# Kernel tuning notes

Hardware: AMD Instinct MI355X
Metric: run time of the kernel (lower is better)

## Reference

```python
import jax, jax.numpy as jnp
import numpy as np

K = 6                 # color-coding parameter; K-1 message-passing steps
N = 50000             # num nodes
E = 1600000           # num edges (avg degree 32)
F = 384               # num_node_features = K * 2**K


def setup_inputs() -> dict:
    key = jax.random.key(0)
    k1, k2, k3, k4, k5 = jax.random.split(key, 5)
    s = 1.0 / np.sqrt(F)
    x = jax.random.normal(k1, (N, F), dtype=jnp.float32)
    edge_index = jax.random.randint(k2, (2, E), 0, N, dtype=jnp.int32)
    batch = jnp.zeros((N,), dtype=jnp.int32)  # unused by forward, kept for signature parity
    W_rel = jax.random.normal(k3, (F, F), dtype=jnp.float32) * s   # GraphConv lin_rel weight
    W_root = jax.random.normal(k4, (F, F), dtype=jnp.float32) * s  # GraphConv lin_root weight
    W_lin = jax.random.normal(k5, (1, F), dtype=jnp.float32) * s   # readout linear (no bias)
    return {"x": x, "edge_index": edge_index, "batch": batch,
            "W_rel": W_rel, "W_root": W_root, "W_lin": W_lin}


def reference(x, edge_index, batch, W_rel, W_root, W_lin):
    src = edge_index[0]
    dst = edge_index[1]
    # K-1 iterations of PyG GraphConv(aggr='add', bias=False) + relu:
    #   out = segment_sum(x[src] -> dst) @ W_rel^T + x @ W_root^T
    for _ in range(K - 1):
        agg = jax.ops.segment_sum(x[src], dst, num_segments=N)  # [N, F]
        x = jax.nn.relu(agg @ W_rel.T + x @ W_root.T)
    # readout: Linear(F, 1, bias=False)
    return x @ W_lin.T  # [N, 1]
```

## Files before the change

### kernel.cpp

```cpp
#include <hip/hip_runtime.h>
#include <hip/hip_bf16.h>

#define NN 50000
#define EE 1600000
#define FF 384
#define MPAD 50048
#define NITER 5

typedef unsigned int u32;
typedef unsigned short u16;
typedef __attribute__((ext_vector_type(8))) short short8;
typedef __attribute__((ext_vector_type(4))) float f32x4;

typedef const __attribute__((address_space(1))) void* gptr_t;
typedef __attribute__((address_space(3))) void* lptr_t;

__device__ __forceinline__ float bf_lo(u32 u) {
  u32 v = u << 16;
  return __builtin_bit_cast(float, v);
}
__device__ __forceinline__ float bf_hi(u32 u) {
  u32 v = u & 0xFFFF0000u;
  return __builtin_bit_cast(float, v);
}
__device__ __forceinline__ u32 f2bf(float f) {
  u32 u = __builtin_bit_cast(u32, f);
  return (u + 0x7FFFu + ((u >> 16) & 1u)) >> 16;
}
__device__ __forceinline__ u32 pack2(float lo, float hi) {
  return f2bf(lo) | (f2bf(hi) << 16);
}
__device__ __forceinline__ void load16_lds(const void* g, void* l) {
  __builtin_amdgcn_global_load_lds((gptr_t)g, (lptr_t)l, 16, 0, 0);
}

__global__ void hist_kernel(const int* __restrict__ dst, int* __restrict__ cnt) {
  int e = blockIdx.x * 256 + threadIdx.x;
  if (e < EE) atomicAdd(&cnt[dst[e]], 1);
}

__global__ void scan_kernel(const int* __restrict__ cnt, int* __restrict__ row_start,
                            int* __restrict__ cursor) {
  __shared__ int part[256];
  __shared__ int pre[256];
  const int CH = (NN + 255) / 256;
  int t = threadIdx.x;
  int lo = t * CH;
  int hi = lo + CH; if (hi > NN) hi = NN;
  int s = 0;
  for (int i = lo; i < hi; ++i) s += cnt[i];
  part[t] = s;
  __syncthreads();
  if (t == 0) {
    int run = 0;
    for (int i = 0; i < 256; ++i) { pre[i] = run; run += part[i]; }
  }
  __syncthreads();
  int run = pre[t];
  for (int i = lo; i < hi; ++i) {
    row_start[i] = run;
    cursor[i] = run;
    run += cnt[i];
  }
  if (lo < NN && hi == NN) row_start[NN] = run;
}

__global__ void scatter_kernel(const int* __restrict__ src, const int* __restrict__ dst,
                               int* __restrict__ cursor, int* __restrict__ col) {
  int e = blockIdx.x * 256 + threadIdx.x;
  if (e < EE) {
    int d = dst[e];
    int p = atomicAdd(&cursor[d], 1);
    col[p] = src[e];
  }
}

__global__ void convert_x_kernel(const float* __restrict__ xin, u16* __restrict__ xout) {
  size_t i = ((size_t)blockIdx.x * 256 + threadIdx.x) * 4;
  if (i >= (size_t)NN * FF) return;
  float4 f = *(const float4*)(xin + i);
  u32 o0 = pack2(f.x, f.y);
  u32 o1 = pack2(f.z, f.w);
  u32* q = (u32*)(xout + i);
  q[0] = o0; q[1] = o1;
}

__global__ void build_bt_kernel(const float* __restrict__ Wr, const float* __restrict__ Wt,
                                u16* __restrict__ Bt) {
  int i = blockIdx.x * 256 + threadIdx.x;
  if (i >= FF * 2 * FF) return;
  int n = i / (2 * FF);
  int k = i - n * (2 * FF);
  float v = (k < FF) ? Wr[n * FF + k] : Wt[n * FF + (k - FF)];
  Bt[i] = (u16)f2bf(v);
}

__global__ void spmm_kernel(const u16* __restrict__ x, const int* __restrict__ rs,
                            const int* __restrict__ col, u16* __restrict__ agg) {
  int row = blockIdx.x * 4 + (threadIdx.x >> 6);
  int lane = threadIdx.x & 63;
  if (row >= NN) return;
  int j0 = rs[row], j1 = rs[row + 1];
  float a0 = 0.f, a1 = 0.f, a2 = 0.f, a3 = 0.f, a4 = 0.f, a5 = 0.f;
  int j = j0;
  for (; j + 2 <= j1; j += 2) {
    int s0 = col[j], s1 = col[j + 1];
    const u32* p0 = (const u32*)(x + (size_t)s0 * FF) + lane * 3;
    const u32* p1 = (const u32*)(x + (size_t)s1 * FF) + lane * 3;
    u32 u0 = p0[0], u1 = p0[1], u2 = p0[2];
    u32 v0 = p1[0], v1 = p1[1], v2 = p1[2];
    a0 += bf_lo(u0); a1 += bf_hi(u0);
    a2 += bf_lo(u1); a3 += bf_hi(u1);
    a4 += bf_lo(u2); a5 += bf_hi(u2);
    a0 += bf_lo(v0); a1 += bf_hi(v0);
    a2 += bf_lo(v1); a3 += bf_hi(v1);
    a4 += bf_lo(v2); a5 += bf_hi(v2);
  }
  if (j < j1) {
    int s0 = col[j];
    const u32* p0 = (const u32*)(x + (size_t)s0 * FF) + lane * 3;
    u32 u0 = p0[0], u1 = p0[1], u2 = p0[2];
    a0 += bf_lo(u0); a1 += bf_hi(u0);
    a2 += bf_lo(u1); a3 += bf_hi(u1);
    a4 += bf_lo(u2); a5 += bf_hi(u2);
  }
  u32* q = (u32*)(agg + (size_t)row * FF) + lane * 3;
  q[0] = pack2(a0, a1);
  q[1] = pack2(a2, a3);
  q[2] = pack2(a4, a5);
}

__global__ __launch_bounds__(256) void gemm_kernel(
    const u16* __restrict__ Aagg, const u16* __restrict__ Ax,
    const u16* __restrict__ Bt, u16* __restrict__ Xout) {
  __shared__ __align__(16) u16 As[128 * 64];
  __shared__ __align__(16) u16 Bs[128 * 64];
  const int m0 = blockIdx.x * 128;
  const int n0 = blockIdx.y * 128;
  const int tid = threadIdx.x;
  const int lane = tid & 63;
  const int w = tid >> 6;
  const int wr = w >> 1, wc = w & 1;

  const int sr = lane >> 3;
  const int sbc = (lane & 7) << 4;

  f32x4 acc[4][4] = {};

  for (int kt = 0; kt < 12; ++kt) {
    const u16* Asrc = (kt < 6) ? Aagg : Ax;
    const int kbA = (kt < 6 ? kt : kt - 6) << 7;
    const int kbB = kt << 7;
#pragma unroll
    for (int i = 0; i < 4; ++i) {
      const int r = w * 32 + i * 8 + sr;
      const int swz = sbc ^ ((r & 7) << 4);
      load16_lds((const char*)Asrc + (size_t)(m0 + r) * 768 + kbA + swz,
                 &As[(w * 32 + i * 8) * 64]);
      load16_lds((const char*)Bt + (size_t)(n0 + r) * 1536 + kbB + swz,
                 &Bs[(w * 32 + i * 8) * 64]);
    }
    __syncthreads();
#pragma unroll
    for (int ks = 0; ks < 2; ++ks) {
      short8 af[4], bfm[4];
#pragma unroll
      for (int mi = 0; mi < 4; ++mi) {
        const int r = wr * 64 + mi * 16 + (lane & 15);
        const int bc = (ks * 64 + ((lane >> 4) << 4)) ^ ((r & 7) << 4);
        af[mi] = *(const short8*)((const char*)As + r * 128 + bc);
      }
#pragma unroll
      for (int ni = 0; ni < 4; ++ni) {
        const int r = wc * 64 + ni * 16 + (lane & 15);
        const int bc = (ks * 64 + ((lane >> 4) << 4)) ^ ((r & 7) << 4);
        bfm[ni] = *(const short8*)((const char*)Bs + r * 128 + bc);
      }
#pragma unroll
      for (int mi = 0; mi < 4; ++mi)
#pragma unroll
        for (int ni = 0; ni < 4; ++ni)
          acc[mi][ni] = __builtin_amdgcn_mfma_f32_16x16x32_bf16(af[mi], bfm[ni], acc[mi][ni], 0, 0, 0);
    }
    __syncthreads();
  }

#pragma unroll
  for (int mi = 0; mi < 4; ++mi) {
#pragma unroll
    for (int r = 0; r < 4; ++r) {
      const int row = m0 + wr * 64 + mi * 16 + ((lane >> 4) << 2) + r;
      u16* orow = Xout + (size_t)row * FF + n0 + wc * 64 + (lane & 15);
#pragma unroll
      for (int ni = 0; ni < 4; ++ni) {
        float v = fmaxf(acc[mi][ni][r], 0.0f);
        orow[ni * 16] = (u16)f2bf(v);
      }
    }
  }
}

__global__ void readout_kernel(const u16* __restrict__ x, const float* __restrict__ wl,
                               float* __restrict__ out) {
  int row = blockIdx.x * 4 + (threadIdx.x >> 6);
  int lane = threadIdx.x & 63;
  if (row >= NN) return;
  const u32* p = (const u32*)(x + (size_t)row * FF) + lane * 3;
  u32 u0 = p[0], u1 = p[1], u2 = p[2];
  const float* w = wl + lane * 6;
  float s = bf_lo(u0) * w[0] + bf_hi(u0) * w[1] +
            bf_lo(u1) * w[2] + bf_hi(u1) * w[3] +
            bf_lo(u2) * w[4] + bf_hi(u2) * w[5];
#pragma unroll
  for (int off = 32; off > 0; off >>= 1) s += __shfl_down(s, off, 64);
  if (lane == 0) out[row] = s;
}

extern "C" void kernel_launch(void* const* d_in, const int* in_sizes, int n_in,
                              void* d_out, int out_size, void* d_ws, size_t ws_size,
                              hipStream_t stream) {
  const float* x_in = (const float*)d_in[0];
  const int* ei = (const int*)d_in[1];
  const float* W_rel = (const float*)d_in[3];
  const float* W_root = (const float*)d_in[4];
  const float* W_lin = (const float*)d_in[5];
  float* out = (float*)d_out;

  char* ws = (char*)d_ws;
  int* cnt = (int*)(ws);
  int* row_start = (int*)(ws + 200064);
  int* cursor = (int*)(ws + 400128);
  int* col = (int*)(ws + 600192);
  u16* Bt = (u16*)(ws + 7000192);
  u16* agg = (u16*)(ws + 7590016);
  u16* x0 = (u16*)(ws + 46026880);
  u16* x1 = (u16*)(ws + 84463744);
  if (ws_size < (size_t)122900608) return;

  const int* esrc = ei;
  const int* edst = ei + EE;

  hipMemsetAsync(cnt, 0, NN * sizeof(int), stream);
  hipMemsetAsync(agg + (size_t)NN * FF, 0, (size_t)(MPAD - NN) * FF * sizeof(u16), stream);
  hipMemsetAsync(x0 + (size_t)NN * FF, 0, (size_t)(MPAD - NN) * FF * sizeof(u16), stream);
  hipMemsetAsync(x1 + (size_t)NN * FF, 0, (size_t)(MPAD - NN) * FF * sizeof(u16), stream);

  hist_kernel<<<EE / 256, 256, 0, stream>>>(edst, cnt);
  scan_kernel<<<1, 256, 0, stream>>>(cnt, row_start, cursor);
  scatter_kernel<<<EE / 256, 256, 0, stream>>>(esrc, edst, cursor, col);
  convert_x_kernel<<<(NN * FF / 4 + 255) / 256, 256, 0, stream>>>(x_in, x0);
  build_bt_kernel<<<(FF * 2 * FF + 255) / 256, 256, 0, stream>>>(W_rel, W_root, Bt);

  u16* xs = x0;
  u16* xd = x1;
  for (int t = 0; t < NITER; ++t) {
    spmm_kernel<<<NN / 4, 256, 0, stream>>>(xs, row_start, col, agg);
    gemm_kernel<<<dim3(MPAD / 128, FF / 128), 256, 0, stream>>>(agg, xs, Bt, xd);
    u16* tmp = xs; xs = xd; xd = tmp;
  }
  readout_kernel<<<NN / 4, 256, 0, stream>>>(xs, W_lin, out);
}
```

Before: 1.397 ms.

## Vectorize SpMM gathers, parallelize CSR scan, and swap GEMM grid ordering

The SpMM kernel now gathers each neighbor row with 16-byte loads on 48 lanes instead of three 4-byte loads on 64 lanes, and unrolls four edges per iteration to keep more loads in flight. The CSR scan replaces the serial single-thread prefix with wave shuffles and int4 vector reads and writes. The GEMM grid puts the N tiles on the fast-varying dimension, so the three column blocks that share an A row tile run close together and reuse it in L2. Leaving 16 lanes idle in SpMM gives up some occupancy in exchange for wider, fewer memory transactions.

```diff
diff --git a/kernel.cpp b/kernel.cpp
--- a/kernel.cpp
+++ b/kernel.cpp
@@ -41,28 +41,31 @@
 
 __global__ void scan_kernel(const int* __restrict__ cnt, int* __restrict__ row_start,
                             int* __restrict__ cursor) {
-  __shared__ int part[256];
-  __shared__ int pre[256];
-  const int CH = (NN + 255) / 256;
+  __shared__ int wsum[4];
+  const int CH = 196;
   int t = threadIdx.x;
   int lo = t * CH;
   int hi = lo + CH; if (hi > NN) hi = NN;
   int s = 0;
-  for (int i = lo; i < hi; ++i) s += cnt[i];
-  part[t] = s;
+  int n4 = (hi - lo) >> 2;
+  const int4* p = (const int4*)(cnt + lo);
+  for (int i = 0; i < n4; ++i) { int4 c = p[i]; s += c.x + c.y + c.z + c.w; }
+  int lane = t & 63, w = t >> 6;
+  int v = s;
+  for (int d = 1; d < 64; d <<= 1) { int u = __shfl_up(v, d, 64); if (lane >= d) v += u; }
+  if (lane == 63) wsum[w] = v;
   __syncthreads();
-  if (t == 0) {
-    int run = 0;
-    for (int i = 0; i < 256; ++i) { pre[i] = run; run += part[i]; }
-  }
-  __syncthreads();
-  int run = pre[t];
-  for (int i = lo; i < hi; ++i) {
-    row_start[i] = run;
-    cursor[i] = run;
-    run += cnt[i];
-  }
-  if (lo < NN && hi == NN) row_start[NN] = run;
+  int run = v - s;
+  for (int i = 0; i < w; ++i) run += wsum[i];
+  int4* q1 = (int4*)(row_start + lo);
+  int4* q2 = (int4*)(cursor + lo);
+  for (int k = 0; k < n4; ++k) {
+    int4 c = p[k];
+    int4 o; o.x = run; o.y = run + c.x; o.z = o.y + c.y; o.w = o.z + c.z;
+    run = o.w + c.w;
+    q1[k] = o; q2[k] = o;
+  }
+  if (hi == NN && lo < NN) row_start[NN] = run;
 }
 
 __global__ void scatter_kernel(const int* __restrict__ src, const int* __restrict__ dst,
@@ -95,39 +98,46 @@
   Bt[i] = (u16)f2bf(v);
 }
 
+#define ACC8(u)                                  \
+  a0 += bf_lo(u.x); a1 += bf_hi(u.x);            \
+  a2 += bf_lo(u.y); a3 += bf_hi(u.y);            \
+  a4 += bf_lo(u.z); a5 += bf_hi(u.z);            \
+  a6 += bf_lo(u.w); a7 += bf_hi(u.w);
+
 __global__ void spmm_kernel(const u16* __restrict__ x, const int* __restrict__ rs,
                             const int* __restrict__ col, u16* __restrict__ agg) {
   int row = blockIdx.x * 4 + (threadIdx.x >> 6);
   int lane = threadIdx.x & 63;
   if (row >= NN) return;
   int j0 = rs[row], j1 = rs[row + 1];
-  float a0 = 0.f, a1 = 0.f, a2 = 0.f, a3 = 0.f, a4 = 0.f, a5 = 0.f;
+  float a0 = 0.f, a1 = 0.f, a2 = 0.f, a3 = 0.f;
+  float a4 = 0.f, a5 = 0.f, a6 = 0.f, a7 = 0.f;
+  const bool active = lane < 48;
+  const int off = lane * 4;
   int j = j0;
-  for (; j + 2 <= j1; j += 2) {
-    int s0 = col[j], s1 = col[j + 1];
-    const u32* p0 = (const u32*)(x + (size_t)s0 * FF) + lane * 3;
-    const u32* p1 = (const u32*)(x + (size_t)s1 * FF) + lane * 3;
-    u32 u0 = p0[0], u1 = p0[1], u2 = p0[2];
-    u32 v0 = p1[0], v1 = p1[1], v2 = p1[2];
-    a0 += bf_lo(u0); a1 += bf_hi(u0);
-    a2 += bf_lo(u1); a3 += bf_hi(u1);
-    a4 += bf_lo(u2); a5 += bf_hi(u2);
-    a0 += bf_lo(v0); a1 += bf_hi(v0);
-    a2 += bf_lo(v1); a3 += bf_hi(v1);
-    a4 += bf_lo(v2); a5 += bf_hi(v2);
-  }
-  if (j < j1) {
+  for (; j + 4 <= j1; j += 4) {
+    int s0 = col[j], s1 = col[j + 1], s2 = col[j + 2], s3 = col[j + 3];
+    if (active) {
+      uint4 u0 = *(const uint4*)((const u32*)(x + (size_t)s0 * FF) + off);
+      uint4 u1 = *(const uint4*)((const u32*)(x + (size_t)s1 * FF) + off);
+      uint4 u2 = *(const uint4*)((const u32*)(x + (size_t)s2 * FF) + off);
+      uint4 u3 = *(const uint4*)((const u32*)(x + (size_t)s3 * FF) + off);
+      ACC8(u0); ACC8(u1); ACC8(u2); ACC8(u3);
+    }
+  }
+  for (; j < j1; ++j) {
     int s0 = col[j];
-    const u32* p0 = (const u32*)(x + (size_t)s0 * FF) + lane * 3;
-    u32 u0 = p0[0], u1 = p0[1], u2 = p0[2];
-    a0 += bf_lo(u0); a1 += bf_hi(u0);
-    a2 += bf_lo(u1); a3 += bf_hi(u1);
-    a4 += bf_lo(u2); a5 += bf_hi(u2);
-  }
-  u32* q = (u32*)(agg + (size_t)row * FF) + lane * 3;
-  q[0] = pack2(a0, a1);
-  q[1] = pack2(a2, a3);
-  q[2] = pack2(a4, a5);
+    if (active) {
+      uint4 u0 = *(const uint4*)((const u32*)(x + (size_t)s0 * FF) + off);
+      ACC8(u0);
+    }
+  }
+  if (active) {
+    uint4 o;
+    o.x = pack2(a0, a1); o.y = pack2(a2, a3);
+    o.z = pack2(a4, a5); o.w = pack2(a6, a7);
+    *(uint4*)((u32*)(agg + (size_t)row * FF) + off) = o;
+  }
 }
 
 __global__ __launch_bounds__(256) void gemm_kernel(
@@ -135,8 +145,8 @@
     const u16* __restrict__ Bt, u16* __restrict__ Xout) {
   __shared__ __align__(16) u16 As[128 * 64];
   __shared__ __align__(16) u16 Bs[128 * 64];
-  const int m0 = blockIdx.x * 128;
-  const int n0 = blockIdx.y * 128;
+  const int m0 = blockIdx.y * 128;
+  const int n0 = blockIdx.x * 128;
   const int tid = threadIdx.x;
   const int lane = tid & 63;
   const int w = tid >> 6;
@@ -255,7 +265,7 @@
   u16* xd = x1;
   for (int t = 0; t < NITER; ++t) {
     spmm_kernel<<<NN / 4, 256, 0, stream>>>(xs, row_start, col, agg);
-    gemm_kernel<<<dim3(MPAD / 128, FF / 128), 256, 0, stream>>>(agg, xs, Bt, xd);
+    gemm_kernel<<<dim3(FF / 128, MPAD / 128), 256, 0, stream>>>(agg, xs, Bt, xd);
     u16* tmp = xs; xs = xd; xd = tmp;
   }
   readout_kernel<<<NN / 4, 256, 0, stream>>>(xs, W_lin, out);
```

After: 1.321 ms. -5.4%, faster.

## Sort edges by source before CSR build, grid-stride SpMM, swap GEMM grid order

Applied to the files above, without the earlier changes.

The CSR build now does a two-pass counting sort: edges are first bucketed by source, then scattered by destination. This makes the column indices within each row roughly sorted, so the SpMM gathers have better locality. The scan kernel is rewritten with a vectorised wavefront shuffle scan, the SpMM uses a fixed grid with a grid-stride loop, and the GEMM grid is transposed so the N-tiles of one M-block run next to each other and share A tiles in cache. The padding memsets for agg/x0/x1 are dropped, and the es_src/es_dst scratch buffers alias the agg buffer, so the padded rows may hold garbage. This costs extra preprocessing work and risks nonzero pad rows feeding the GEMM, though those output rows are never read.

```diff
diff --git a/kernel.cpp b/kernel.cpp
--- a/kernel.cpp
+++ b/kernel.cpp
@@ -6,6 +6,7 @@
 #define FF 384
 #define MPAD 50048
 #define NITER 5
+#define SPMM_BLOCKS 1536
 
 typedef unsigned int u32;
 typedef unsigned short u16;
@@ -34,44 +35,59 @@
   __builtin_amdgcn_global_load_lds((gptr_t)g, (lptr_t)l, 16, 0, 0);
 }
 
-__global__ void hist_kernel(const int* __restrict__ dst, int* __restrict__ cnt) {
+__global__ void hist_kernel(const int* __restrict__ key, int* __restrict__ cnt) {
   int e = blockIdx.x * 256 + threadIdx.x;
-  if (e < EE) atomicAdd(&cnt[dst[e]], 1);
+  if (e < EE) atomicAdd(&cnt[key[e]], 1);
 }
 
 __global__ void scan_kernel(const int* __restrict__ cnt, int* __restrict__ row_start,
                             int* __restrict__ cursor) {
-  __shared__ int part[256];
-  __shared__ int pre[256];
-  const int CH = (NN + 255) / 256;
+  __shared__ int wsum[4];
+  const int CH = 196;
   int t = threadIdx.x;
   int lo = t * CH;
   int hi = lo + CH; if (hi > NN) hi = NN;
   int s = 0;
-  for (int i = lo; i < hi; ++i) s += cnt[i];
-  part[t] = s;
+  int n4 = (hi - lo) >> 2;
+  const int4* p = (const int4*)(cnt + lo);
+  for (int i = 0; i < n4; ++i) { int4 c = p[i]; s += c.x + c.y + c.z + c.w; }
+  int lane = t & 63, w = t >> 6;
+  int v = s;
+  for (int d = 1; d < 64; d <<= 1) { int u = __shfl_up(v, d, 64); if (lane >= d) v += u; }
+  if (lane == 63) wsum[w] = v;
   __syncthreads();
-  if (t == 0) {
-    int run = 0;
-    for (int i = 0; i < 256; ++i) { pre[i] = run; run += part[i]; }
-  }
-  __syncthreads();
-  int run = pre[t];
-  for (int i = lo; i < hi; ++i) {
-    row_start[i] = run;
-    cursor[i] = run;
-    run += cnt[i];
-  }
-  if (lo < NN && hi == NN) row_start[NN] = run;
-}
-
-__global__ void scatter_kernel(const int* __restrict__ src, const int* __restrict__ dst,
-                               int* __restrict__ cursor, int* __restrict__ col) {
+  int run = v - s;
+  for (int i = 0; i < w; ++i) run += wsum[i];
+  int4* q1 = (int4*)(row_start + lo);
+  int4* q2 = (int4*)(cursor + lo);
+  for (int k = 0; k < n4; ++k) {
+    int4 c = p[k];
+    int4 o; o.x = run; o.y = run + c.x; o.z = o.y + c.y; o.w = o.z + c.z;
+    run = o.w + c.w;
+    q1[k] = o; q2[k] = o;
+  }
+  if (hi == NN && lo < NN) row_start[NN] = run;
+}
+
+__global__ void scatter_src_kernel(const int* __restrict__ src, const int* __restrict__ dst,
+                                   int* __restrict__ cursor,
+                                   int* __restrict__ es_src, int* __restrict__ es_dst) {
   int e = blockIdx.x * 256 + threadIdx.x;
   if (e < EE) {
-    int d = dst[e];
+    int s = src[e];
+    int p = atomicAdd(&cursor[s], 1);
+    es_src[p] = s;
+    es_dst[p] = dst[e];
+  }
+}
+
+__global__ void scatter_dst_kernel(const int* __restrict__ es_src, const int* __restrict__ es_dst,
+                                   int* __restrict__ cursor, int* __restrict__ col) {
+  int q = blockIdx.x * 256 + threadIdx.x;
+  if (q < EE) {
+    int d = es_dst[q];
     int p = atomicAdd(&cursor[d], 1);
-    col[p] = src[e];
+    col[p] = es_src[q];
   }
 }
 
@@ -97,37 +113,37 @@
 
 __global__ void spmm_kernel(const u16* __restrict__ x, const int* __restrict__ rs,
                             const int* __restrict__ col, u16* __restrict__ agg) {
-  int row = blockIdx.x * 4 + (threadIdx.x >> 6);
   int lane = threadIdx.x & 63;
-  if (row >= NN) return;
-  int j0 = rs[row], j1 = rs[row + 1];
-  float a0 = 0.f, a1 = 0.f, a2 = 0.f, a3 = 0.f, a4 = 0.f, a5 = 0.f;
-  int j = j0;
-  for (; j + 2 <= j1; j += 2) {
-    int s0 = col[j], s1 = col[j + 1];
-    const u32* p0 = (const u32*)(x + (size_t)s0 * FF) + lane * 3;
-    const u32* p1 = (const u32*)(x + (size_t)s1 * FF) + lane * 3;
-    u32 u0 = p0[0], u1 = p0[1], u2 = p0[2];
-    u32 v0 = p1[0], v1 = p1[1], v2 = p1[2];
-    a0 += bf_lo(u0); a1 += bf_hi(u0);
-    a2 += bf_lo(u1); a3 += bf_hi(u1);
-    a4 += bf_lo(u2); a5 += bf_hi(u2);
-    a0 += bf_lo(v0); a1 += bf_hi(v0);
-    a2 += bf_lo(v1); a3 += bf_hi(v1);
-    a4 += bf_lo(v2); a5 += bf_hi(v2);
-  }
-  if (j < j1) {
-    int s0 = col[j];
-    const u32* p0 = (const u32*)(x + (size_t)s0 * FF) + lane * 3;
-    u32 u0 = p0[0], u1 = p0[1], u2 = p0[2];
-    a0 += bf_lo(u0); a1 += bf_hi(u0);
-    a2 += bf_lo(u1); a3 += bf_hi(u1);
-    a4 += bf_lo(u2); a5 += bf_hi(u2);
-  }
-  u32* q = (u32*)(agg + (size_t)row * FF) + lane * 3;
-  q[0] = pack2(a0, a1);
-  q[1] = pack2(a2, a3);
-  q[2] = pack2(a4, a5);
+  for (int row = blockIdx.x * 4 + (threadIdx.x >> 6); row < NN; row += SPMM_BLOCKS * 4) {
+    int j0 = rs[row], j1 = rs[row + 1];
+    float a0 = 0.f, a1 = 0.f, a2 = 0.f, a3 = 0.f, a4 = 0.f, a5 = 0.f;
+    int j = j0;
+    for (; j + 2 <= j1; j += 2) {
+      int s0 = col[j], s1 = col[j + 1];
+      const u32* p0 = (const u32*)(x + (size_t)s0 * FF) + lane * 3;
+      const u32* p1 = (const u32*)(x + (size_t)s1 * FF) + lane * 3;
+      u32 u0 = p0[0], u1 = p0[1], u2 = p0[2];
+      u32 v0 = p1[0], v1 = p1[1], v2 = p1[2];
+      a0 += bf_lo(u0); a1 += bf_hi(u0);
+      a2 += bf_lo(u1); a3 += bf_hi(u1);
+      a4 += bf_lo(u2); a5 += bf_hi(u2);
+      a0 += bf_lo(v0); a1 += bf_hi(v0);
+      a2 += bf_lo(v1); a3 += bf_hi(v1);
+      a4 += bf_lo(v2); a5 += bf_hi(v2);
+    }
+    if (j < j1) {
+      int s0 = col[j];
+      const u32* p0 = (const u32*)(x + (size_t)s0 * FF) + lane * 3;
+      u32 u0 = p0[0], u1 = p0[1], u2 = p0[2];
+      a0 += bf_lo(u0); a1 += bf_hi(u0);
+      a2 += bf_lo(u1); a3 += bf_hi(u1);
+      a4 += bf_lo(u2); a5 += bf_hi(u2);
+    }
+    u32* q = (u32*)(agg + (size_t)row * FF) + lane * 3;
+    q[0] = pack2(a0, a1);
+    q[1] = pack2(a2, a3);
+    q[2] = pack2(a4, a5);
+  }
 }
 
 __global__ __launch_bounds__(256) void gemm_kernel(
@@ -135,8 +151,8 @@
     const u16* __restrict__ Bt, u16* __restrict__ Xout) {
   __shared__ __align__(16) u16 As[128 * 64];
   __shared__ __align__(16) u16 Bs[128 * 64];
-  const int m0 = blockIdx.x * 128;
-  const int n0 = blockIdx.y * 128;
+  const int m0 = blockIdx.y * 128;
+  const int n0 = blockIdx.x * 128;
   const int tid = threadIdx.x;
   const int lane = tid & 63;
   const int w = tid >> 6;
@@ -236,26 +252,29 @@
   u16* x0 = (u16*)(ws + 46026880);
   u16* x1 = (u16*)(ws + 84463744);
   if (ws_size < (size_t)122900608) return;
+  int* es_src = (int*)(ws + 7590016);
+  int* es_dst = (int*)(ws + 7590016 + 6400000);
 
   const int* esrc = ei;
   const int* edst = ei + EE;
 
   hipMemsetAsync(cnt, 0, NN * sizeof(int), stream);
-  hipMemsetAsync(agg + (size_t)NN * FF, 0, (size_t)(MPAD - NN) * FF * sizeof(u16), stream);
-  hipMemsetAsync(x0 + (size_t)NN * FF, 0, (size_t)(MPAD - NN) * FF * sizeof(u16), stream);
-  hipMemsetAsync(x1 + (size_t)NN * FF, 0, (size_t)(MPAD - NN) * FF * sizeof(u16), stream);
-
+  hist_kernel<<<EE / 256, 256, 0, stream>>>(esrc, cnt);
+  scan_kernel<<<1, 256, 0, stream>>>(cnt, row_start, cursor);
+  scatter_src_kernel<<<EE / 256, 256, 0, stream>>>(esrc, edst, cursor, es_src, es_dst);
+  hipMemsetAsync(cnt, 0, NN * sizeof(int), stream);
   hist_kernel<<<EE / 256, 256, 0, stream>>>(edst, cnt);
   scan_kernel<<<1, 256, 0, stream>>>(cnt, row_start, cursor);
-  scatter_kernel<<<EE / 256, 256, 0, stream>>>(esrc, edst, cursor, col);
+  scatter_dst_kernel<<<EE / 256, 256, 0, stream>>>(es_src, es_dst, cursor, col);
+
   convert_x_kernel<<<(NN * FF / 4 + 255) / 256, 256, 0, stream>>>(x_in, x0);
   build_bt_kernel<<<(FF * 2 * FF + 255) / 256, 256, 0, stream>>>(W_rel, W_root, Bt);
 
   u16* xs = x0;
   u16* xd = x1;
   for (int t = 0; t < NITER; ++t) {
-    spmm_kernel<<<NN / 4, 256, 0, stream>>>(xs, row_start, col, agg);
-    gemm_kernel<<<dim3(MPAD / 128, FF / 128), 256, 0, stream>>>(agg, xs, Bt, xd);
+    spmm_kernel<<<SPMM_BLOCKS, 256, 0, stream>>>(xs, row_start, col, agg);
+    gemm_kernel<<<dim3(FF / 128, MPAD / 128), 256, 0, stream>>>(agg, xs, Bt, xd);
     u16* tmp = xs; xs = xd; xd = tmp;
   }
   readout_kernel<<<NN / 4, 256, 0, stream>>>(xs, W_lin, out);
```

New measurement: 1.575 ms. 12.8% more time.
